# Performance work log

Hardware: AMD Instinct MI355X
Metric: run time of the kernel (lower is better)

## Reference

```python
import jax, jax.numpy as jnp
import numpy as np

N = 100000
IN_DIM = 128
HID = 256
OUT_DIM = 128
E = 600000


def setup_inputs() -> dict:
    key = jax.random.key(0)
    ks = jax.random.split(key, 10)
    x = jax.random.normal(ks[0], (N, IN_DIM), dtype=jnp.float32)
    edge_index = jax.random.randint(ks[1], (2, E), 0, N, dtype=jnp.int32)

    def lin(k, fan_in, fan_out):
        kw, kb = jax.random.split(k)
        bound = 1.0 / np.sqrt(fan_in)
        W = jax.random.uniform(kw, (fan_in, fan_out), minval=-bound, maxval=bound, dtype=jnp.float32)
        b = jax.random.uniform(kb, (fan_out,), minval=-bound, maxval=bound, dtype=jnp.float32)
        return W, b

    W1a, b1a = lin(ks[2], IN_DIM, HID)
    W1b, b1b = lin(ks[3], HID, HID)
    W2a, b2a = lin(ks[4], HID, HID)
    W2b, b2b = lin(ks[5], HID, OUT_DIM)
    return {"x": x, "edge_index": edge_index,
            "W1a": W1a, "b1a": b1a, "W1b": W1b, "b1b": b1b,
            "W2a": W2a, "b2a": b2a, "W2b": W2b, "b2b": b2b}


def _gin_conv(x, src, dst, Wa, ba, Wb, bb):
    # GINConv with eps=0: h = (1+eps)*x + sum_{j in N(i)} x_j, then 2-layer MLP
    agg = jax.ops.segment_sum(x[src], dst, num_segments=N)  # [N, F]
    h = x + agg
    h = jax.nn.relu(h @ Wa + ba)
    return h @ Wb + bb


def reference(x, edge_index, W1a, b1a, W1b, b1b, W2a, b2a, W2b, b2b):
    src, dst = edge_index[0], edge_index[1]
    h = jax.nn.relu(_gin_conv(x, src, dst, W1a, b1a, W1b, b1b))
    h = jax.nn.relu(_gin_conv(h, src, dst, W2a, b2a, W2b, b2b))
    return h
```

## Files before the change

kernel.cpp:

```cpp
#include <hip/hip_runtime.h>
#include <stdint.h>

#define N_NODES 100000
#define E_EDGES 600000
#define IN_F    128
#define HID_F   256
#define OUT_F   128
#define NB_SCAN 98

typedef unsigned short ushort_t;
typedef short  short8  __attribute__((ext_vector_type(8)));
typedef float  floatx4 __attribute__((ext_vector_type(4)));

__device__ __forceinline__ float bf2f(unsigned u16) {
    return __uint_as_float(u16 << 16);
}
__device__ __forceinline__ ushort_t f2bf(float f) {
    unsigned u = __float_as_uint(f);
    return (ushort_t)((u + 0x7fffu + ((u >> 16) & 1u)) >> 16);
}

__global__ void k_prep(const float* __restrict__ x, ushort_t* __restrict__ xbf,
                       const float* __restrict__ W1a, const float* __restrict__ W1b,
                       const float* __restrict__ W2a, const float* __restrict__ W2b,
                       ushort_t* __restrict__ WT1a, ushort_t* __restrict__ WT1b,
                       ushort_t* __restrict__ WT2a, ushort_t* __restrict__ WT2b,
                       int* __restrict__ cursor, ushort_t* __restrict__ P) {
    int t = blockIdx.x * 256 + threadIdx.x;
    if (t < N_NODES * IN_F / 2) {
        float2 v = ((const float2*)x)[t];
        ((unsigned*)xbf)[t] = (unsigned)f2bf(v.x) | ((unsigned)f2bf(v.y) << 16);
    }
    if (t < N_NODES) cursor[t] = 0;
    if (t < 128) ((unsigned*)(P + (size_t)N_NODES * HID_F))[t] = 0;
    if (t < 64)  ((unsigned*)(xbf + (size_t)N_NODES * IN_F))[t] = 0;
    if (t < 32768) {
        int k = t >> 8, n = t & 255;
        WT1a[n * 128 + k] = f2bf(W1a[t]);
    } else if (t < 98304) {
        int i = t - 32768, k = i >> 8, n = i & 255;
        WT1b[n * 256 + k] = f2bf(W1b[i]);
    } else if (t < 163840) {
        int i = t - 98304, k = i >> 8, n = i & 255;
        WT2a[n * 256 + k] = f2bf(W2a[i]);
    } else if (t < 196608) {
        int i = t - 163840, k = i >> 7, n = i & 127;
        WT2b[n * 256 + k] = f2bf(W2b[i]);
    }
}

__global__ void k_hist(const int* __restrict__ dst, int* __restrict__ deg) {
    int e = blockIdx.x * 256 + threadIdx.x;
    if (e < E_EDGES) atomicAdd(&deg[dst[e]], 1);
}

__global__ void k_scan1(const int* __restrict__ deg, int* __restrict__ row_ptr,
                        int* __restrict__ psum) {
    __shared__ int s[1024];
    int t = threadIdx.x, i = blockIdx.x * 1024 + t;
    int v = (i < N_NODES) ? deg[i] : 0;
    s[t] = v;
    __syncthreads();
    for (int off = 1; off < 1024; off <<= 1) {
        int u = (t >= off) ? s[t - off] : 0;
        __syncthreads();
        if (t >= off) s[t] += u;
        __syncthreads();
    }
    if (i < N_NODES) row_ptr[i] = s[t] - v;
    if (t == 1023) psum[blockIdx.x] = s[t];
}

__global__ void k_scan2(int* __restrict__ psum) {
    __shared__ int s[128];
    int t = threadIdx.x;
    int v = (t < NB_SCAN) ? psum[t] : 0;
    s[t] = v;
    __syncthreads();
    for (int off = 1; off < 128; off <<= 1) {
        int u = (t >= off) ? s[t - off] : 0;
        __syncthreads();
        if (t >= off) s[t] += u;
        __syncthreads();
    }
    if (t < NB_SCAN) psum[t] = s[t] - v;
}

__global__ void k_scan3(int* __restrict__ row_ptr, const int* __restrict__ psum,
                        int* __restrict__ cursor) {
    int i = blockIdx.x * 1024 + threadIdx.x;
    if (i < N_NODES) {
        int r = row_ptr[i] + psum[i >> 10];
        row_ptr[i] = r;
        cursor[i]  = r;
    }
    if (i == 0) row_ptr[N_NODES] = E_EDGES;
}

__global__ void k_fill(const int* __restrict__ src, const int* __restrict__ dst,
                       int* __restrict__ cursor, int* __restrict__ colidx) {
    int e = blockIdx.x * 256 + threadIdx.x;
    if (e < E_EDGES) {
        int pos = atomicAdd(&cursor[dst[e]], 1);
        colidx[pos] = src[e];
    }
}

__global__ void k_agg128(const ushort_t* __restrict__ Xbf, const int* __restrict__ row_ptr,
                         const int* __restrict__ colidx, ushort_t* __restrict__ Out) {
    int node = blockIdx.x * 4 + (threadIdx.x >> 6);
    int lane = threadIdx.x & 63;
    int q = lane >> 4, l4 = lane & 15;
    const uint4* xr = (const uint4*)Xbf;
    uint4 u = xr[(size_t)node * 16 + l4];
    float a0 = q ? 0.f : bf2f(u.x & 0xffffu);
    float a1 = q ? 0.f : bf2f(u.x >> 16);
    float a2 = q ? 0.f : bf2f(u.y & 0xffffu);
    float a3 = q ? 0.f : bf2f(u.y >> 16);
    float a4 = q ? 0.f : bf2f(u.z & 0xffffu);
    float a5 = q ? 0.f : bf2f(u.z >> 16);
    float a6 = q ? 0.f : bf2f(u.w & 0xffffu);
    float a7 = q ? 0.f : bf2f(u.w >> 16);
    int r0 = row_ptr[node], r1 = row_ptr[node + 1];
    for (int base = r0 + q; base < r1; base += 8) {
        int j0 = colidx[base];
        int j1 = colidx[min(base + 4, r1 - 1)];
        j1 = (base + 4 < r1) ? j1 : N_NODES;
        uint4 w0 = xr[(size_t)j0 * 16 + l4];
        uint4 w1 = xr[(size_t)j1 * 16 + l4];
        a0 += bf2f(w0.x & 0xffffu) + bf2f(w1.x & 0xffffu);
        a1 += bf2f(w0.x >> 16)     + bf2f(w1.x >> 16);
        a2 += bf2f(w0.y & 0xffffu) + bf2f(w1.y & 0xffffu);
        a3 += bf2f(w0.y >> 16)     + bf2f(w1.y >> 16);
        a4 += bf2f(w0.z & 0xffffu) + bf2f(w1.z & 0xffffu);
        a5 += bf2f(w0.z >> 16)     + bf2f(w1.z >> 16);
        a6 += bf2f(w0.w & 0xffffu) + bf2f(w1.w & 0xffffu);
        a7 += bf2f(w0.w >> 16)     + bf2f(w1.w >> 16);
    }
    a0 += __shfl_xor(a0, 16, 64); a0 += __shfl_xor(a0, 32, 64);
    a1 += __shfl_xor(a1, 16, 64); a1 += __shfl_xor(a1, 32, 64);
    a2 += __shfl_xor(a2, 16, 64); a2 += __shfl_xor(a2, 32, 64);
    a3 += __shfl_xor(a3, 16, 64); a3 += __shfl_xor(a3, 32, 64);
    a4 += __shfl_xor(a4, 16, 64); a4 += __shfl_xor(a4, 32, 64);
    a5 += __shfl_xor(a5, 16, 64); a5 += __shfl_xor(a5, 32, 64);
    a6 += __shfl_xor(a6, 16, 64); a6 += __shfl_xor(a6, 32, 64);
    a7 += __shfl_xor(a7, 16, 64); a7 += __shfl_xor(a7, 32, 64);
    if (q == 0) {
        uint4 o;
        o.x = (unsigned)f2bf(a0) | ((unsigned)f2bf(a1) << 16);
        o.y = (unsigned)f2bf(a2) | ((unsigned)f2bf(a3) << 16);
        o.z = (unsigned)f2bf(a4) | ((unsigned)f2bf(a5) << 16);
        o.w = (unsigned)f2bf(a6) | ((unsigned)f2bf(a7) << 16);
        ((uint4*)Out)[(size_t)node * 16 + l4] = o;
    }
}

__global__ void k_agg256(const ushort_t* __restrict__ X, const int* __restrict__ row_ptr,
                         const int* __restrict__ colidx, ushort_t* __restrict__ Out) {
    int node = blockIdx.x * 4 + (threadIdx.x >> 6);
    int lane = threadIdx.x & 63;
    int h = lane >> 5, l5 = lane & 31;
    const uint4* xr = (const uint4*)X;
    uint4 u = xr[(size_t)node * 32 + l5];
    float a0 = h ? 0.f : bf2f(u.x & 0xffffu);
    float a1 = h ? 0.f : bf2f(u.x >> 16);
    float a2 = h ? 0.f : bf2f(u.y & 0xffffu);
    float a3 = h ? 0.f : bf2f(u.y >> 16);
    float a4 = h ? 0.f : bf2f(u.z & 0xffffu);
    float a5 = h ? 0.f : bf2f(u.z >> 16);
    float a6 = h ? 0.f : bf2f(u.w & 0xffffu);
    float a7 = h ? 0.f : bf2f(u.w >> 16);
    int r0 = row_ptr[node], r1 = row_ptr[node + 1];
    for (int base = r0 + h; base < r1; base += 8) {
        int j0 = colidx[base];
        int j1 = colidx[min(base + 2, r1 - 1)];
        int j2 = colidx[min(base + 4, r1 - 1)];
        int j3 = colidx[min(base + 6, r1 - 1)];
        j1 = (base + 2 < r1) ? j1 : N_NODES;
        j2 = (base + 4 < r1) ? j2 : N_NODES;
        j3 = (base + 6 < r1) ? j3 : N_NODES;
        uint4 w0 = xr[(size_t)j0 * 32 + l5];
        uint4 w1 = xr[(size_t)j1 * 32 + l5];
        uint4 w2 = xr[(size_t)j2 * 32 + l5];
        uint4 w3 = xr[(size_t)j3 * 32 + l5];
        a0 += (bf2f(w0.x & 0xffffu) + bf2f(w1.x & 0xffffu)) +
              (bf2f(w2.x & 0xffffu) + bf2f(w3.x & 0xffffu));
        a1 += (bf2f(w0.x >> 16) + bf2f(w1.x >> 16)) +
              (bf2f(w2.x >> 16) + bf2f(w3.x >> 16));
        a2 += (bf2f(w0.y & 0xffffu) + bf2f(w1.y & 0xffffu)) +
              (bf2f(w2.y & 0xffffu) + bf2f(w3.y & 0xffffu));
        a3 += (bf2f(w0.y >> 16) + bf2f(w1.y >> 16)) +
              (bf2f(w2.y >> 16) + bf2f(w3.y >> 16));
        a4 += (bf2f(w0.z & 0xffffu) + bf2f(w1.z & 0xffffu)) +
              (bf2f(w2.z & 0xffffu) + bf2f(w3.z & 0xffffu));
        a5 += (bf2f(w0.z >> 16) + bf2f(w1.z >> 16)) +
              (bf2f(w2.z >> 16) + bf2f(w3.z >> 16));
        a6 += (bf2f(w0.w & 0xffffu) + bf2f(w1.w & 0xffffu)) +
              (bf2f(w2.w & 0xffffu) + bf2f(w3.w & 0xffffu));
        a7 += (bf2f(w0.w >> 16) + bf2f(w1.w >> 16)) +
              (bf2f(w2.w >> 16) + bf2f(w3.w >> 16));
    }
    a0 += __shfl_xor(a0, 32, 64);
    a1 += __shfl_xor(a1, 32, 64);
    a2 += __shfl_xor(a2, 32, 64);
    a3 += __shfl_xor(a3, 32, 64);
    a4 += __shfl_xor(a4, 32, 64);
    a5 += __shfl_xor(a5, 32, 64);
    a6 += __shfl_xor(a6, 32, 64);
    a7 += __shfl_xor(a7, 32, 64);
    if (h == 0) {
        uint4 o;
        o.x = (unsigned)f2bf(a0) | ((unsigned)f2bf(a1) << 16);
        o.y = (unsigned)f2bf(a2) | ((unsigned)f2bf(a3) << 16);
        o.z = (unsigned)f2bf(a4) | ((unsigned)f2bf(a5) << 16);
        o.w = (unsigned)f2bf(a6) | ((unsigned)f2bf(a7) << 16);
        ((uint4*)Out)[(size_t)node * 32 + l5] = o;
    }
}

template <int FIN, int FOUT, bool OUT_F32>
__global__ __launch_bounds__(512, 4) void gemm_relu(
    const ushort_t* __restrict__ Act, const ushort_t* __restrict__ WT,
    const float* __restrict__ bias, void* __restrict__ Out, int nRows)
{
    constexpr int CPR = FIN / 8;
    constexpr int KC  = FIN / 32;
    constexpr int KP  = KC / 2;
    constexpr int SW  = 136;
    constexpr int WTE = 128 * FIN;
    constexpr int EPE = 128 * SW;
    __shared__ ushort_t wt[(WTE > EPE) ? WTE : EPE];

    const int tid  = threadIdx.x;
    const int bid  = blockIdx.x;

    int rowblk, sl;
    if (FOUT == 256) {
        const int group = bid >> 4, w = bid & 15;
        rowblk = group * 8 + (w & 7);
        sl     = w >> 3;
        if (rowblk >= (nRows + 255) / 256) return;
    } else {
        rowblk = bid;
        sl     = 0;
    }
    const int slab = sl * 128;

    {
        const ushort_t* wsrc = WT + (size_t)slab * FIN;
#pragma unroll
        for (int rr = 0; rr < (128 * CPR) / 512; ++rr) {
            int ci  = rr * 512 + tid;
            int n   = ci / CPR;
            int csw = ci % CPR;
            int cor = csw ^ (n & 15);
            const ushort_t* g = wsrc + (size_t)n * FIN + cor * 8;
            __builtin_amdgcn_global_load_lds(
                (const __attribute__((address_space(1))) unsigned*)g,
                (__attribute__((address_space(3))) unsigned*)&wt[ci * 8],
                16, 0, 0);
        }
    }

    const int wave = tid >> 6, lane = tid & 63;
    const int quad = lane >> 4, l15 = lane & 15;
    const int rowBase = rowblk * 256 + wave * 32;

    int r0 = rowBase + l15;
    int r1 = r0 + 16;
    r0 = (r0 < nRows) ? r0 : (nRows - 1);
    r1 = (r1 < nRows) ? r1 : (nRows - 1);
    const ushort_t* a0p = Act + (size_t)r0 * FIN + quad * 8;
    const ushort_t* a1p = Act + (size_t)r1 * FIN + quad * 8;

    short8 af[2][2][2];
#pragma unroll
    for (int kc = 0; kc < 2; ++kc) {
        af[0][0][kc] = *(const short8*)(a0p + kc * 32);
        af[0][1][kc] = *(const short8*)(a1p + kc * 32);
    }

    floatx4 acc[2][8];
#pragma unroll
    for (int mt = 0; mt < 2; ++mt)
#pragma unroll
        for (int nt = 0; nt < 8; ++nt)
#pragma unroll
            for (int r = 0; r < 4; ++r) acc[mt][nt][r] = 0.f;

    __syncthreads();

#pragma unroll
    for (int p = 0; p < KP; ++p) {
        const int cb = p & 1, nb = cb ^ 1;
        if (p + 1 < KP) {
#pragma unroll
            for (int kc = 0; kc < 2; ++kc) {
                af[nb][0][kc] = *(const short8*)(a0p + ((p + 1) * 2 + kc) * 32);
                af[nb][1][kc] = *(const short8*)(a1p + ((p + 1) * 2 + kc) * 32);
            }
        }
#pragma unroll
        for (int kc = 0; kc < 2; ++kc) {
            int chunk = (p * 2 + kc) * 4 + quad;
#pragma unroll
            for (int nt = 0; nt < 8; ++nt) {
                int n = nt * 16 + l15;
                int csw = chunk ^ (n & 15);
                short8 bfr = *(const short8*)&wt[n * FIN + csw * 8];
                acc[0][nt] = __builtin_amdgcn_mfma_f32_16x16x32_bf16(af[cb][0][kc], bfr, acc[0][nt], 0, 0, 0);
                acc[1][nt] = __builtin_amdgcn_mfma_f32_16x16x32_bf16(af[cb][1][kc], bfr, acc[1][nt], 0, 0, 0);
            }
        }
    }

    if (!OUT_F32) {
        const int rowTileBase = rowblk * 256;
#pragma unroll
        for (int mt = 0; mt < 2; ++mt) {
            __syncthreads();
#pragma unroll
            for (int nt = 0; nt < 8; ++nt) {
                int col = slab + nt * 16 + l15;
                float bv = bias[col];
#pragma unroll
                for (int r = 0; r < 4; ++r) {
                    float v = fmaxf(acc[mt][nt][r] + bv, 0.f);
                    wt[(wave * 16 + quad * 4 + r) * SW + nt * 16 + l15] = f2bf(v);
                }
            }
            __syncthreads();
#pragma unroll
            for (int it = 0; it < 4; ++it) {
                int idx = it * 512 + tid;
                int gr  = idx >> 4;
                int c   = idx & 15;
                int row = rowTileBase + (gr >> 4) * 32 + mt * 16 + (gr & 15);
                uint4 vv = *(const uint4*)&wt[gr * SW + c * 8];
                if (row < nRows)
                    *(uint4*)((ushort_t*)Out + (size_t)row * FOUT + slab + c * 8) = vv;
            }
        }
    } else {
#pragma unroll
        for (int mt = 0; mt < 2; ++mt) {
#pragma unroll
            for (int nt = 0; nt < 8; ++nt) {
                int col = slab + nt * 16 + l15;
                float bv = bias[col];
#pragma unroll
                for (int r = 0; r < 4; ++r) {
                    int row = rowBase + mt * 16 + quad * 4 + r;
                    if (row < nRows) {
                        float v = fmaxf(acc[mt][nt][r] + bv, 0.f);
                        ((float*)Out)[(size_t)row * FOUT + col] = v;
                    }
                }
            }
        }
    }
}

extern "C" void kernel_launch(void* const* d_in, const int* in_sizes, int n_in,
                              void* d_out, int out_size, void* d_ws, size_t ws_size,
                              hipStream_t stream) {
    const float* x   = (const float*)d_in[0];
    const int*   ei  = (const int*)d_in[1];
    const int*   src = ei;
    const int*   dst = ei + E_EDGES;
    const float* W1a = (const float*)d_in[2];
    const float* b1a = (const float*)d_in[3];
    const float* W1b = (const float*)d_in[4];
    const float* b1b = (const float*)d_in[5];
    const float* W2a = (const float*)d_in[6];
    const float* b2a = (const float*)d_in[7];
    const float* W2b = (const float*)d_in[8];
    const float* b2b = (const float*)d_in[9];

    const size_t NP1 = N_NODES + 1;
    ushort_t* P       = (ushort_t*)d_ws;
    ushort_t* Q       = P + NP1 * HID_F;
    ushort_t* xbf     = Q;
    int*      row_ptr = (int*)(Q + NP1 * HID_F);
    int*      cursor  = row_ptr + (N_NODES + 4);
    int*      colidx  = cursor + N_NODES;
    int*      psum    = colidx + E_EDGES;
    ushort_t* WT1a    = (ushort_t*)(psum + 128);
    ushort_t* WT1b    = WT1a + 256 * 128;
    ushort_t* WT2a    = WT1b + 256 * 256;
    ushort_t* WT2b    = WT2a + 256 * 256;

    k_prep<<<(N_NODES * IN_F / 2 + 255) / 256, 256, 0, stream>>>(
        x, xbf, W1a, W1b, W2a, W2b, WT1a, WT1b, WT2a, WT2b, cursor, P);

    k_hist <<<(E_EDGES + 255) / 256, 256, 0, stream>>>(dst, cursor);
    k_scan1<<<NB_SCAN, 1024, 0, stream>>>(cursor, row_ptr, psum);
    k_scan2<<<1, 128, 0, stream>>>(psum);
    k_scan3<<<NB_SCAN, 1024, 0, stream>>>(row_ptr, psum, cursor);
    k_fill <<<(E_EDGES + 255) / 256, 256, 0, stream>>>(src, dst, cursor, colidx);

    const int ROWB = (N_NODES + 255) / 256;
    const int GP   = ((ROWB + 7) / 8) * 16;

    k_agg128<<<N_NODES / 4, 256, 0, stream>>>(xbf, row_ptr, colidx, P);
    gemm_relu<128, 256, false><<<GP, 512, 0, stream>>>(P, WT1a, b1a, Q, N_NODES);
    gemm_relu<256, 256, false><<<GP, 512, 0, stream>>>(Q, WT1b, b1b, P, N_NODES);

    k_agg256<<<N_NODES / 4, 256, 0, stream>>>(P, row_ptr, colidx, Q);
    gemm_relu<256, 256, false><<<GP, 512, 0, stream>>>(Q, WT2a, b2a, P, N_NODES);
    gemm_relu<256, 128, true><<<ROWB, 512, 0, stream>>>(P, WT2b, b2b, d_out, N_NODES);
}
```

Measured before the change: 368.4 us.

## Fuse CSR build into one persistent kernel with grid barriers and decoupled-lookback scan

Replaces the five-kernel CSR build (histogram, three scan stages, fill) with a single 98-block persistent kernel. Spin-wait grid barriers on a global counter separate the phases, and block prefixes are published through flag-tagged 64-bit slots. The goal is to remove four launch gaps and their small-kernel tail overheads. The catch is that the atomic histogram and fill phases now run on only 98 blocks, and correctness depends on all 98 blocks being co-resident.

```diff
diff --git a/kernel.cpp b/kernel.cpp
--- a/kernel.cpp
+++ b/kernel.cpp
@@ -25,7 +25,8 @@
                        const float* __restrict__ W2a, const float* __restrict__ W2b,
                        ushort_t* __restrict__ WT1a, ushort_t* __restrict__ WT1b,
                        ushort_t* __restrict__ WT2a, ushort_t* __restrict__ WT2b,
-                       int* __restrict__ cursor, ushort_t* __restrict__ P) {
+                       int* __restrict__ cursor, ushort_t* __restrict__ P,
+                       unsigned long long* __restrict__ pub, int* __restrict__ bar) {
     int t = blockIdx.x * 256 + threadIdx.x;
     if (t < N_NODES * IN_F / 2) {
         float2 v = ((const float2*)x)[t];
@@ -34,6 +35,8 @@
     if (t < N_NODES) cursor[t] = 0;
     if (t < 128) ((unsigned*)(P + (size_t)N_NODES * HID_F))[t] = 0;
     if (t < 64)  ((unsigned*)(xbf + (size_t)N_NODES * IN_F))[t] = 0;
+    if (t < 128) pub[t] = 0ull;
+    if (t == 128) bar[0] = 0;
     if (t < 32768) {
         int k = t >> 8, n = t & 255;
         WT1a[n * 128 + k] = f2bf(W1a[t]);
@@ -49,16 +52,29 @@
     }
 }
 
-__global__ void k_hist(const int* __restrict__ dst, int* __restrict__ deg) {
-    int e = blockIdx.x * 256 + threadIdx.x;
-    if (e < E_EDGES) atomicAdd(&deg[dst[e]], 1);
-}
-
-__global__ void k_scan1(const int* __restrict__ deg, int* __restrict__ row_ptr,
-                        int* __restrict__ psum) {
+__global__ void k_csr(const int* __restrict__ src, const int* __restrict__ dst,
+                      int* __restrict__ deg , int* __restrict__ row_ptr,
+                      int* __restrict__ colidx, unsigned long long* __restrict__ pub,
+                      int* __restrict__ bar) {
+    const int t    = threadIdx.x;
+    const int bid  = blockIdx.x;
+    const int gtid = bid * 1024 + t;
+
+    for (int e = gtid; e < E_EDGES; e += NB_SCAN * 1024)
+        atomicAdd(&deg[dst[e]], 1);
+
+    __syncthreads();
+    if (t == 0) {
+        __threadfence();
+        atomicAdd(bar, 1);
+        while (atomicAdd(bar, 0) < NB_SCAN) {}
+    }
+    __syncthreads();
+
     __shared__ int s[1024];
-    int t = threadIdx.x, i = blockIdx.x * 1024 + t;
-    int v = (i < N_NODES) ? deg[i] : 0;
+    __shared__ int pr[1024];
+    int i = gtid;
+    int v = (i < N_NODES) ? atomicAdd(&deg[i], 0) : 0;
     s[t] = v;
     __syncthreads();
     for (int off = 1; off < 1024; off <<= 1) {
@@ -67,41 +83,40 @@
         if (t >= off) s[t] += u;
         __syncthreads();
     }
-    if (i < N_NODES) row_ptr[i] = s[t] - v;
-    if (t == 1023) psum[blockIdx.x] = s[t];
-}
-
-__global__ void k_scan2(int* __restrict__ psum) {
-    __shared__ int s[128];
-    int t = threadIdx.x;
-    int v = (t < NB_SCAN) ? psum[t] : 0;
-    s[t] = v;
-    __syncthreads();
-    for (int off = 1; off < 128; off <<= 1) {
-        int u = (t >= off) ? s[t - off] : 0;
+    if (t == 1023) {
+        __threadfence();
+        atomicExch(&pub[bid], ((unsigned long long)s[1023] << 1) | 1ull);
+    }
+    int part = 0;
+    if (t < bid) {
+        unsigned long long pv;
+        while (((pv = atomicAdd(&pub[t], 0ull)) & 1ull) == 0ull) {}
+        part = (int)(pv >> 1);
+    }
+    pr[t] = part;
+    __syncthreads();
+    for (int off = 512; off > 0; off >>= 1) {
+        if (t < off) pr[t] += pr[t + off];
         __syncthreads();
-        if (t >= off) s[t] += u;
-        __syncthreads();
-    }
-    if (t < NB_SCAN) psum[t] = s[t] - v;
-}
-
-__global__ void k_scan3(int* __restrict__ row_ptr, const int* __restrict__ psum,
-                        int* __restrict__ cursor) {
-    int i = blockIdx.x * 1024 + threadIdx.x;
+    }
+    const int pre = pr[0];
     if (i < N_NODES) {
-        int r = row_ptr[i] + psum[i >> 10];
+        int r = s[t] - v + pre;
         row_ptr[i] = r;
-        cursor[i]  = r;
-    }
-    if (i == 0) row_ptr[N_NODES] = E_EDGES;
-}
-
-__global__ void k_fill(const int* __restrict__ src, const int* __restrict__ dst,
-                       int* __restrict__ cursor, int* __restrict__ colidx) {
-    int e = blockIdx.x * 256 + threadIdx.x;
-    if (e < E_EDGES) {
-        int pos = atomicAdd(&cursor[dst[e]], 1);
+        atomicExch(&deg[i], r);
+    }
+    if (gtid == 0) row_ptr[N_NODES] = E_EDGES;
+
+    __syncthreads();
+    if (t == 0) {
+        __threadfence();
+        atomicAdd(bar, 1);
+        while (atomicAdd(bar, 0) < 2 * NB_SCAN) {}
+    }
+    __syncthreads();
+
+    for (int e = gtid; e < E_EDGES; e += NB_SCAN * 1024) {
+        int pos = atomicAdd(&deg[dst[e]], 1);
         colidx[pos] = src[e];
     }
 }
@@ -384,20 +399,17 @@
     int*      row_ptr = (int*)(Q + NP1 * HID_F);
     int*      cursor  = row_ptr + (N_NODES + 4);
     int*      colidx  = cursor + N_NODES;
-    int*      psum    = colidx + E_EDGES;
-    ushort_t* WT1a    = (ushort_t*)(psum + 128);
+    unsigned long long* pub = (unsigned long long*)(colidx + E_EDGES);
+    int*      bar     = (int*)(pub + 128);
+    ushort_t* WT1a    = (ushort_t*)(bar + 4);
     ushort_t* WT1b    = WT1a + 256 * 128;
     ushort_t* WT2a    = WT1b + 256 * 256;
     ushort_t* WT2b    = WT2a + 256 * 256;
 
     k_prep<<<(N_NODES * IN_F / 2 + 255) / 256, 256, 0, stream>>>(
-        x, xbf, W1a, W1b, W2a, W2b, WT1a, WT1b, WT2a, WT2b, cursor, P);
-
-    k_hist <<<(E_EDGES + 255) / 256, 256, 0, stream>>>(dst, cursor);
-    k_scan1<<<NB_SCAN, 1024, 0, stream>>>(cursor, row_ptr, psum);
-    k_scan2<<<1, 128, 0, stream>>>(psum);
-    k_scan3<<<NB_SCAN, 1024, 0, stream>>>(row_ptr, psum, cursor);
-    k_fill <<<(E_EDGES + 255) / 256, 256, 0, stream>>>(src, dst, cursor, colidx);
+        x, xbf, W1a, W1b, W2a, W2b, WT1a, WT1b, WT2a, WT2b, cursor, P, pub, bar);
+
+    k_csr<<<NB_SCAN, 1024, 0, stream>>>(src, dst, cursor, row_ptr, colidx, pub, bar);
 
     const int ROWB = (N_NODES + 255) / 256;
     const int GP   = ((ROWB + 7) / 8) * 16;
```

After: 383.5 us. +4.1%, slower.
